# Optimization experiments

Hardware: AMD Instinct MI355X
Metric: run time of the kernel (lower is better)

The kernel has to match this reference:

```python
import jax, jax.numpy as jnp
import numpy as np

B, QN, KN, DIN, DPROJ = 8, 2048, 2048, 1024, 1024

def setup_inputs() -> dict:
    key = jax.random.key(0)
    ks = jax.random.split(key, 10)
    s = 1.0 / np.sqrt(DIN)
    return {
        "query": jax.random.normal(ks[0], (B, QN, DIN), jnp.float32),
        "key": jax.random.normal(ks[1], (B, KN, DIN), jnp.float32),
        "value": jax.random.normal(ks[2], (B, KN, DIN), jnp.float32),
        "mask": jax.random.randint(ks[3], (B, KN), 0, 2, jnp.int32),
        "Wq": jax.random.uniform(ks[4], (DPROJ, DIN), jnp.float32, -s, s),
        "bq": jax.random.uniform(ks[5], (DPROJ,), jnp.float32, -s, s),
        "Wk": jax.random.uniform(ks[6], (DPROJ, DIN), jnp.float32, -s, s),
        "bk": jax.random.uniform(ks[7], (DPROJ,), jnp.float32, -s, s),
        "Wv": jax.random.uniform(ks[8], (DPROJ, DIN), jnp.float32, -s, s),
        "bv": jax.random.uniform(ks[9], (DPROJ,), jnp.float32, -s, s),
    }

def reference(query, key, value, mask, Wq, bq, Wk, bk, Wv, bv):
    pq = jnp.einsum('bqc,dc->bqd', query, Wq) + bq  # (b, qn, dproj)
    pk = jnp.einsum('bkc,dc->bkd', key, Wk) + bk    # (b, kn, dproj)
    pv = jnp.einsum('bkc,dc->bkd', value, Wv) + bv  # (b, kn, dproj)
    scores = jnp.einsum('bqd,bkd->bqk', pq, pk) / jnp.sqrt(jnp.float32(DPROJ))
    m = mask[:, None, :]  # (b, 1, kn) broadcasts over qn
    scores = jnp.where(m == 0, jnp.float32(-1e9), scores)
    attn = jax.nn.softmax(scores, axis=-1)
    attn = attn * m.astype(attn.dtype)  # post-softmax double mask
    ctx = jnp.einsum('bqk,bkd->bqd', attn, pv)
    return (ctx, attn)
```

## Files before the change

### kernel.cpp

```cpp
#include <hip/hip_runtime.h>
#include <hip/hip_bf16.h>


typedef __bf16 bf16;
typedef __bf16 bf16x4 __attribute__((ext_vector_type(4)));
typedef __bf16 bf16x8 __attribute__((ext_vector_type(8)));
typedef float f32x4 __attribute__((ext_vector_type(4)));

#define BAR() asm volatile("s_barrier" ::: "memory")
#define WAIT_LGKM0() do { asm volatile("s_waitcnt lgkmcnt(0)" ::: "memory"); \
                          __builtin_amdgcn_sched_barrier(0); } while (0)

__device__ __forceinline__ void gld_lds16(const bf16* g, bf16* l) {
  __builtin_amdgcn_global_load_lds(
      (const __attribute__((address_space(1))) void*)g,
      (__attribute__((address_space(3))) void*)l, 16, 0, 0);
}

__global__ __launch_bounds__(256)
void cvt_f32_bf16(const float* __restrict__ src, bf16* __restrict__ dst, int n)
{
  long i = ((long)blockIdx.x * 256 + threadIdx.x) * 8;
  if (i >= n) return;
  f32x4 a = *(const f32x4*)&src[i];
  f32x4 b = *(const f32x4*)&src[i + 4];
  bf16x8 o;
  o[0] = (bf16)a[0]; o[1] = (bf16)a[1]; o[2] = (bf16)a[2]; o[3] = (bf16)a[3];
  o[4] = (bf16)b[0]; o[5] = (bf16)b[1]; o[6] = (bf16)b[2]; o[7] = (bf16)b[3];
  *(bf16x8*)&dst[i] = o;
}

__global__ __launch_bounds__(512, 2)
void gemm8p(const bf16* __restrict__ A, int lda, long sA,
            const bf16* __restrict__ Bt, int ldb, long sB,
            void* __restrict__ Cout, int ldc, long sC, int c_bf16,
            const float* __restrict__ bias, int bias_mode,
            int K, float scale)
{
  extern __shared__ bf16 lds[];
  const int tid = threadIdx.x;
  const int lane = tid & 63;
  const int wid = tid >> 6;
  const int wr = wid >> 2;
  const int wc = wid & 3;
  const long m0 = (long)blockIdx.x * 256;
  const long n0 = (long)blockIdx.y * 256;
  A  += (long)blockIdx.z * sA;
  Bt += (long)blockIdx.z * sB;

  const int fr = lane & 15, fq = lane >> 4;
  const int cs0 = (((fq * 16)      ^ ((fr & 7) << 4)) >> 1);
  const int cs1 = (((64 + fq * 16) ^ ((fr & 7) << 4)) >> 1);
  const int rbA = (wr * 128 + fr) * 64;
  const int rbB = 16384 + (wc * 64 + fr) * 64;

  const int srow = tid >> 3;
  const int slot = (tid & 7) ^ (srow & 7);
  const bf16* Ag[4]; const bf16* Bg[4];
#pragma unroll
  for (int h = 0; h < 2; ++h)
#pragma unroll
    for (int i = 0; i < 2; ++i) {
      Ag[h * 2 + i] = A  + (m0 + h * 128 + i * 64 + srow) * (long)lda + slot * 8;
      Bg[h * 2 + i] = Bt + (n0 + h * 128 + i * 64 + srow) * (long)ldb + slot * 8;
    }
  const int ldst = tid * 8;

  const int NT = K >> 6;
  f32x4 acc[8][4] = {};

#pragma unroll
  for (int hi = 0; hi < 4; ++hi)
    gld_lds16(Ag[hi], &lds[(hi >> 1) * 8192 + (hi & 1) * 4096 + ldst]);
#pragma unroll
  for (int hi = 0; hi < 4; ++hi)
    gld_lds16(Bg[hi], &lds[16384 + (hi >> 1) * 8192 + (hi & 1) * 4096 + ldst]);
#pragma unroll
  for (int hi = 0; hi < 4; ++hi)
    gld_lds16(Bg[hi] + 64, &lds[49152 + (hi >> 1) * 8192 + (hi & 1) * 4096 + ldst]);
  asm volatile("s_waitcnt vmcnt(4)" ::: "memory");
  BAR();

  for (int t = 0; t < NT; ++t) {
    const int bo  = (t & 1) << 15;
    const int nbo = bo ^ 32768;
    const int kof  = (t + 1) * 64;
    const int kof2 = (t + 2) * 64;
    const bool st1 = (t + 1 < NT), st2 = (t + 2 < NT);

    bf16x8 a0[4][2], b0[2][2], b1[2][2];

#pragma unroll
    for (int mf = 0; mf < 4; ++mf) {
      a0[mf][0] = *(const bf16x8*)&lds[bo + rbA + mf * 1024 + cs0];
      a0[mf][1] = *(const bf16x8*)&lds[bo + rbA + mf * 1024 + cs1];
    }
#pragma unroll
    for (int nf = 0; nf < 2; ++nf) {
      b0[nf][0] = *(const bf16x8*)&lds[bo + rbB + nf * 1024 + cs0];
      b0[nf][1] = *(const bf16x8*)&lds[bo + rbB + nf * 1024 + cs1];
    }
    if (st1) {
      gld_lds16(Ag[0] + kof, &lds[nbo + ldst]);
      gld_lds16(Ag[1] + kof, &lds[nbo + 4096 + ldst]);
    }
    BAR(); WAIT_LGKM0();
    __builtin_amdgcn_s_setprio(1);
#pragma unroll
    for (int mf = 0; mf < 4; ++mf)
#pragma unroll
      for (int nf = 0; nf < 2; ++nf) {
        acc[mf][nf] = __builtin_amdgcn_mfma_f32_16x16x32_bf16(a0[mf][0], b0[nf][0], acc[mf][nf], 0, 0, 0);
        acc[mf][nf] = __builtin_amdgcn_mfma_f32_16x16x32_bf16(a0[mf][1], b0[nf][1], acc[mf][nf], 0, 0, 0);
      }
    __builtin_amdgcn_s_setprio(0);
    BAR();

#pragma unroll
    for (int nf = 0; nf < 2; ++nf) {
      b1[nf][0] = *(const bf16x8*)&lds[bo + rbB + (nf + 2) * 1024 + cs0];
      b1[nf][1] = *(const bf16x8*)&lds[bo + rbB + (nf + 2) * 1024 + cs1];
    }
    if (st1) {
      gld_lds16(Ag[2] + kof, &lds[nbo + 8192 + ldst]);
      gld_lds16(Ag[3] + kof, &lds[nbo + 8192 + 4096 + ldst]);
    }
    BAR(); WAIT_LGKM0();
    __builtin_amdgcn_s_setprio(1);
#pragma unroll
    for (int mf = 0; mf < 4; ++mf)
#pragma unroll
      for (int nf = 0; nf < 2; ++nf) {
        acc[mf][nf + 2] = __builtin_amdgcn_mfma_f32_16x16x32_bf16(a0[mf][0], b1[nf][0], acc[mf][nf + 2], 0, 0, 0);
        acc[mf][nf + 2] = __builtin_amdgcn_mfma_f32_16x16x32_bf16(a0[mf][1], b1[nf][1], acc[mf][nf + 2], 0, 0, 0);
      }
    __builtin_amdgcn_s_setprio(0);
    BAR();

#pragma unroll
    for (int mf = 0; mf < 4; ++mf) {
      a0[mf][0] = *(const bf16x8*)&lds[bo + rbA + (mf + 4) * 1024 + cs0];
      a0[mf][1] = *(const bf16x8*)&lds[bo + rbA + (mf + 4) * 1024 + cs1];
    }
    if (st2) {
      gld_lds16(Bg[0] + kof2, &lds[bo + 16384 + ldst]);
      gld_lds16(Bg[1] + kof2, &lds[bo + 16384 + 4096 + ldst]);
    }
    BAR(); WAIT_LGKM0();
    __builtin_amdgcn_s_setprio(1);
#pragma unroll
    for (int mf = 0; mf < 4; ++mf)
#pragma unroll
      for (int nf = 0; nf < 2; ++nf) {
        acc[mf + 4][nf + 2] = __builtin_amdgcn_mfma_f32_16x16x32_bf16(a0[mf][0], b1[nf][0], acc[mf + 4][nf + 2], 0, 0, 0);
        acc[mf + 4][nf + 2] = __builtin_amdgcn_mfma_f32_16x16x32_bf16(a0[mf][1], b1[nf][1], acc[mf + 4][nf + 2], 0, 0, 0);
      }
    __builtin_amdgcn_s_setprio(0);
    BAR();

    if (st2) {
      gld_lds16(Bg[2] + kof2, &lds[bo + 16384 + 8192 + ldst]);
      gld_lds16(Bg[3] + kof2, &lds[bo + 16384 + 8192 + 4096 + ldst]);
      asm volatile("s_waitcnt vmcnt(4)" ::: "memory");
    } else {
      asm volatile("s_waitcnt vmcnt(0)" ::: "memory");
    }
    BAR(); WAIT_LGKM0();
    __builtin_amdgcn_s_setprio(1);
#pragma unroll
    for (int mf = 0; mf < 4; ++mf)
#pragma unroll
      for (int nf = 0; nf < 2; ++nf) {
        acc[mf + 4][nf] = __builtin_amdgcn_mfma_f32_16x16x32_bf16(a0[mf][0], b0[nf][0], acc[mf + 4][nf], 0, 0, 0);
        acc[mf + 4][nf] = __builtin_amdgcn_mfma_f32_16x16x32_bf16(a0[mf][1], b0[nf][1], acc[mf + 4][nf], 0, 0, 0);
      }
    __builtin_amdgcn_s_setprio(0);
    BAR();
  }

  const int cc = lane & 15, cq = lane >> 4;
  const long crow0 = m0 + wr * 128;
  const long ccol0 = n0 + wc * 64;
  if (c_bf16) {
    bf16* C = (bf16*)Cout + (long)blockIdx.z * sC;
#pragma unroll
    for (int mf = 0; mf < 8; ++mf)
#pragma unroll
      for (int nf = 0; nf < 4; ++nf)
#pragma unroll
        for (int r = 0; r < 4; ++r) {
          long row = crow0 + mf * 16 + cq * 4 + r;
          long col = ccol0 + nf * 16 + cc;
          float v = acc[mf][nf][r] * scale;
          if (bias_mode == 1) v += bias[col];
          else if (bias_mode == 2) v += bias[row];
          C[row * (long)ldc + col] = (bf16)v;
        }
  } else {
    float* C = (float*)Cout + (long)blockIdx.z * sC;
#pragma unroll
    for (int mf = 0; mf < 8; ++mf)
#pragma unroll
      for (int nf = 0; nf < 4; ++nf)
#pragma unroll
        for (int r = 0; r < 4; ++r) {
          long row = crow0 + mf * 16 + cq * 4 + r;
          long col = ccol0 + nf * 16 + cc;
          float v = acc[mf][nf][r] * scale;
          if (bias_mode == 1) v += bias[col];
          else if (bias_mode == 2) v += bias[row];
          C[row * (long)ldc + col] = v;
        }
  }
}

__global__ __launch_bounds__(256)
void softmax_mask(const int* __restrict__ mask, float* __restrict__ attn,
                  bf16* __restrict__ attnb)
{
  const int row = blockIdx.x;
  const int b = row >> 11;
  float* arow = attn + (long)row * 2048;
  const bf16* srow_b = (const bf16*)arow;
  bf16* brow = attnb + (long)row * 2048;
  const int* mrow = mask + (b << 11);
  const int tid = threadIdx.x;
  const int lane = tid & 63, wave = tid >> 6;

  bf16x4 sb[2];
  int4 mk[2];
  sb[0] = *(const bf16x4*)&srow_b[tid * 4];
  sb[1] = *(const bf16x4*)&srow_b[1024 + tid * 4];
  mk[0] = *(const int4*)&mrow[tid * 4];
  mk[1] = *(const int4*)&mrow[1024 + tid * 4];
  const int m[8] = {mk[0].x, mk[0].y, mk[0].z, mk[0].w,
                    mk[1].x, mk[1].y, mk[1].z, mk[1].w};
  float s[8];
#pragma unroll
  for (int i = 0; i < 8; ++i) s[i] = (float)sb[i >> 2][i & 3];

  float mx = -3e38f;
#pragma unroll
  for (int i = 0; i < 8; ++i)
    if (m[i]) mx = fmaxf(mx, s[i]);
#pragma unroll
  for (int off = 32; off > 0; off >>= 1) mx = fmaxf(mx, __shfl_xor(mx, off));
  __shared__ float rmax[4], rsum[4];
  if (lane == 0) rmax[wave] = mx;
  __syncthreads();
  mx = fmaxf(fmaxf(rmax[0], rmax[1]), fmaxf(rmax[2], rmax[3]));

  float e[8], sum = 0.f;
#pragma unroll
  for (int i = 0; i < 8; ++i) {
    e[i] = m[i] ? __expf(s[i] - mx) : 0.f;
    sum += e[i];
  }
#pragma unroll
  for (int off = 32; off > 0; off >>= 1) sum += __shfl_xor(sum, off);
  if (lane == 0) rsum[wave] = sum;
  __syncthreads();
  sum = rsum[0] + rsum[1] + rsum[2] + rsum[3];
  float inv = sum > 0.f ? 1.f / sum : 0.f;

  f32x4 o; bf16x4 ob;
#pragma unroll
  for (int h = 0; h < 2; ++h) {
#pragma unroll
    for (int i = 0; i < 4; ++i) {
      float v = e[h * 4 + i] * inv;
      o[i] = v; ob[i] = (bf16)v;
    }
    *(f32x4*)&arow[h * 1024 + tid * 4] = o;
    *(bf16x4*)&brow[h * 1024 + tid * 4] = ob;
  }
}

extern "C" void kernel_launch(void* const* d_in, const int* in_sizes, int n_in,
                              void* d_out, int out_size, void* d_ws, size_t ws_size,
                              hipStream_t stream)
{
  const float* query = (const float*)d_in[0];
  const float* key   = (const float*)d_in[1];
  const float* value = (const float*)d_in[2];
  const int*   mask  = (const int*)d_in[3];
  const float* Wq = (const float*)d_in[4];
  const float* bq = (const float*)d_in[5];
  const float* Wk = (const float*)d_in[6];
  const float* bk = (const float*)d_in[7];
  const float* Wv = (const float*)d_in[8];
  const float* bv = (const float*)d_in[9];

  float* ctx  = (float*)d_out;
  float* attn = ctx + (size_t)8 * 2048 * 1024;

  bf16* Pq    = (bf16*)d_ws;
  bf16* Pk    = Pq + (size_t)16384 * 1024;
  bf16* PvT   = Pk + (size_t)16384 * 1024;
  bf16* attnb = (bf16*)d_ws;

  bf16* qb  = (bf16*)attn;
  bf16* kb  = qb + (size_t)16384 * 1024;
  bf16* vb  = kb + (size_t)16384 * 1024;
  bf16* Wqb = vb + (size_t)16384 * 1024;
  bf16* Wkb = Wqb + (size_t)1024 * 1024;
  bf16* Wvb = Wkb + (size_t)1024 * 1024;

  static bool attr_set = false;
  if (!attr_set) {
    hipFuncSetAttribute(reinterpret_cast<const void*>(gemm8p),
                        hipFuncAttributeMaxDynamicSharedMemorySize, 131072);
    attr_set = true;
  }

  dim3 blk(256), blk8(512);

  hipLaunchKernelGGL(cvt_f32_bf16, dim3(8192), blk, 0, stream, query, qb, 16384 * 1024);
  hipLaunchKernelGGL(cvt_f32_bf16, dim3(8192), blk, 0, stream, key,   kb, 16384 * 1024);
  hipLaunchKernelGGL(cvt_f32_bf16, dim3(8192), blk, 0, stream, value, vb, 16384 * 1024);
  hipLaunchKernelGGL(cvt_f32_bf16, dim3(512),  blk, 0, stream, Wq, Wqb, 1024 * 1024);
  hipLaunchKernelGGL(cvt_f32_bf16, dim3(512),  blk, 0, stream, Wk, Wkb, 1024 * 1024);
  hipLaunchKernelGGL(cvt_f32_bf16, dim3(512),  blk, 0, stream, Wv, Wvb, 1024 * 1024);

  hipLaunchKernelGGL(gemm8p, dim3(64, 4, 1), blk8, 131072, stream,
      qb, 1024, 0L, Wqb, 1024, 0L, (void*)Pq, 1024, 0L, 1, bq, 1, 1024, 1.0f);
  hipLaunchKernelGGL(gemm8p, dim3(64, 4, 1), blk8, 131072, stream,
      kb, 1024, 0L, Wkb, 1024, 0L, (void*)Pk, 1024, 0L, 1, bk, 1, 1024, 1.0f);
  hipLaunchKernelGGL(gemm8p, dim3(4, 64, 1), blk8, 131072, stream,
      Wvb, 1024, 0L, vb, 1024, 0L, (void*)PvT, 16384, 0L, 1, bv, 2, 1024, 1.0f);
  hipLaunchKernelGGL(gemm8p, dim3(8, 8, 8), blk8, 131072, stream,
      Pq, 1024, (long)2048 * 1024, Pk, 1024, (long)2048 * 1024,
      (void*)attn, 4096, (long)2048 * 4096, 1, (const float*)nullptr, 0, 1024, 0.03125f);
  hipLaunchKernelGGL(softmax_mask, dim3(16384), blk, 0, stream, mask, attn, attnb);
  hipLaunchKernelGGL(gemm8p, dim3(8, 4, 8), blk8, 131072, stream,
      attnb, 2048, (long)2048 * 2048, PvT, 16384, 2048L,
      (void*)ctx, 1024, (long)2048 * 1024, 0, (const float*)nullptr, 0, 2048, 1.0f);
}
```

Baseline: 681.7 us.

## Restructure GEMM main loop into two phases and merge conversion launches

The GEMM K-loop goes from four barrier-separated MFMA phases to two. Each phase loads all four A or B fragment pairs, issues all four half-tile global-to-LDS prefetches at once, and waits partially on lgkmcnt before the barrier. This cuts barriers and gives longer MFMA runs, at the cost of more live fragment registers under the 512-thread, 2-block occupancy bound. The six fp32-to-bf16 conversion launches are merged into one kernel that dispatches on a flat index, removing launch overhead.

```diff
diff --git a/kernel.cpp b/kernel.cpp
--- a/kernel.cpp
+++ b/kernel.cpp
@@ -17,17 +17,30 @@
       (__attribute__((address_space(3))) void*)l, 16, 0, 0);
 }
 
-__global__ __launch_bounds__(256)
-void cvt_f32_bf16(const float* __restrict__ src, bf16* __restrict__ dst, int n)
-{
-  long i = ((long)blockIdx.x * 256 + threadIdx.x) * 8;
-  if (i >= n) return;
-  f32x4 a = *(const f32x4*)&src[i];
-  f32x4 b = *(const f32x4*)&src[i + 4];
+__device__ __forceinline__ void cvt8(const float* s, bf16* d, long i) {
+  f32x4 a = *(const f32x4*)&s[i];
+  f32x4 b = *(const f32x4*)&s[i + 4];
   bf16x8 o;
   o[0] = (bf16)a[0]; o[1] = (bf16)a[1]; o[2] = (bf16)a[2]; o[3] = (bf16)a[3];
   o[4] = (bf16)b[0]; o[5] = (bf16)b[1]; o[6] = (bf16)b[2]; o[7] = (bf16)b[3];
-  *(bf16x8*)&dst[i] = o;
+  *(bf16x8*)&d[i] = o;
+}
+
+__global__ __launch_bounds__(256)
+void cvt_all(const float* __restrict__ s0, bf16* __restrict__ d0, long n0,
+             const float* __restrict__ s1, bf16* __restrict__ d1, long n1,
+             const float* __restrict__ s2, bf16* __restrict__ d2, long n2,
+             const float* __restrict__ s3, bf16* __restrict__ d3, long n3,
+             const float* __restrict__ s4, bf16* __restrict__ d4, long n4,
+             const float* __restrict__ s5, bf16* __restrict__ d5, long n5)
+{
+  long g = ((long)blockIdx.x * 256 + threadIdx.x) * 8;
+  if (g < n0) { cvt8(s0, d0, g); return; } g -= n0;
+  if (g < n1) { cvt8(s1, d1, g); return; } g -= n1;
+  if (g < n2) { cvt8(s2, d2, g); return; } g -= n2;
+  if (g < n3) { cvt8(s3, d3, g); return; } g -= n3;
+  if (g < n4) { cvt8(s4, d4, g); return; } g -= n4;
+  if (g < n5) { cvt8(s5, d5, g); return; }
 }
 
 __global__ __launch_bounds__(512, 2)
@@ -58,12 +71,10 @@
   const int slot = (tid & 7) ^ (srow & 7);
   const bf16* Ag[4]; const bf16* Bg[4];
 #pragma unroll
-  for (int h = 0; h < 2; ++h)
-#pragma unroll
-    for (int i = 0; i < 2; ++i) {
-      Ag[h * 2 + i] = A  + (m0 + h * 128 + i * 64 + srow) * (long)lda + slot * 8;
-      Bg[h * 2 + i] = Bt + (n0 + h * 128 + i * 64 + srow) * (long)ldb + slot * 8;
-    }
+  for (int hi = 0; hi < 4; ++hi) {
+    Ag[hi] = A  + (m0 + hi * 64 + srow) * (long)lda + slot * 8;
+    Bg[hi] = Bt + (n0 + hi * 64 + srow) * (long)ldb + slot * 8;
+  }
   const int ldst = tid * 8;
 
   const int NT = K >> 6;
@@ -71,13 +82,13 @@
 
 #pragma unroll
   for (int hi = 0; hi < 4; ++hi)
-    gld_lds16(Ag[hi], &lds[(hi >> 1) * 8192 + (hi & 1) * 4096 + ldst]);
+    gld_lds16(Ag[hi], &lds[hi * 4096 + ldst]);
 #pragma unroll
   for (int hi = 0; hi < 4; ++hi)
-    gld_lds16(Bg[hi], &lds[16384 + (hi >> 1) * 8192 + (hi & 1) * 4096 + ldst]);
+    gld_lds16(Bg[hi], &lds[16384 + hi * 4096 + ldst]);
 #pragma unroll
   for (int hi = 0; hi < 4; ++hi)
-    gld_lds16(Bg[hi] + 64, &lds[49152 + (hi >> 1) * 8192 + (hi & 1) * 4096 + ldst]);
+    gld_lds16(Bg[hi] + 64, &lds[49152 + hi * 4096 + ldst]);
   asm volatile("s_waitcnt vmcnt(4)" ::: "memory");
   BAR();
 
@@ -88,79 +99,47 @@
     const int kof2 = (t + 2) * 64;
     const bool st1 = (t + 1 < NT), st2 = (t + 2 < NT);
 
-    bf16x8 a0[4][2], b0[2][2], b1[2][2];
-
+    bf16x8 a[4][2], b[4][2];
+
+    if (st1) {
+#pragma unroll
+      for (int hi = 0; hi < 4; ++hi)
+        gld_lds16(Ag[hi] + kof, &lds[nbo + hi * 4096 + ldst]);
+    }
 #pragma unroll
     for (int mf = 0; mf < 4; ++mf) {
-      a0[mf][0] = *(const bf16x8*)&lds[bo + rbA + mf * 1024 + cs0];
-      a0[mf][1] = *(const bf16x8*)&lds[bo + rbA + mf * 1024 + cs1];
-    }
-#pragma unroll
-    for (int nf = 0; nf < 2; ++nf) {
-      b0[nf][0] = *(const bf16x8*)&lds[bo + rbB + nf * 1024 + cs0];
-      b0[nf][1] = *(const bf16x8*)&lds[bo + rbB + nf * 1024 + cs1];
-    }
-    if (st1) {
-      gld_lds16(Ag[0] + kof, &lds[nbo + ldst]);
-      gld_lds16(Ag[1] + kof, &lds[nbo + 4096 + ldst]);
-    }
+      a[mf][0] = *(const bf16x8*)&lds[bo + rbA + mf * 1024 + cs0];
+      a[mf][1] = *(const bf16x8*)&lds[bo + rbA + mf * 1024 + cs1];
+    }
+#pragma unroll
+    for (int nf = 0; nf < 4; ++nf) {
+      b[nf][0] = *(const bf16x8*)&lds[bo + rbB + nf * 1024 + cs0];
+      b[nf][1] = *(const bf16x8*)&lds[bo + rbB + nf * 1024 + cs1];
+    }
+    asm volatile("s_waitcnt lgkmcnt(8)" ::: "memory");
     BAR(); WAIT_LGKM0();
     __builtin_amdgcn_s_setprio(1);
 #pragma unroll
     for (int mf = 0; mf < 4; ++mf)
 #pragma unroll
-      for (int nf = 0; nf < 2; ++nf) {
-        acc[mf][nf] = __builtin_amdgcn_mfma_f32_16x16x32_bf16(a0[mf][0], b0[nf][0], acc[mf][nf], 0, 0, 0);
-        acc[mf][nf] = __builtin_amdgcn_mfma_f32_16x16x32_bf16(a0[mf][1], b0[nf][1], acc[mf][nf], 0, 0, 0);
+      for (int nf = 0; nf < 4; ++nf) {
+        acc[mf][nf] = __builtin_amdgcn_mfma_f32_16x16x32_bf16(a[mf][0], b[nf][0], acc[mf][nf], 0, 0, 0);
+        acc[mf][nf] = __builtin_amdgcn_mfma_f32_16x16x32_bf16(a[mf][1], b[nf][1], acc[mf][nf], 0, 0, 0);
       }
     __builtin_amdgcn_s_setprio(0);
     BAR();
 
-#pragma unroll
-    for (int nf = 0; nf < 2; ++nf) {
-      b1[nf][0] = *(const bf16x8*)&lds[bo + rbB + (nf + 2) * 1024 + cs0];
-      b1[nf][1] = *(const bf16x8*)&lds[bo + rbB + (nf + 2) * 1024 + cs1];
-    }
-    if (st1) {
-      gld_lds16(Ag[2] + kof, &lds[nbo + 8192 + ldst]);
-      gld_lds16(Ag[3] + kof, &lds[nbo + 8192 + 4096 + ldst]);
-    }
-    BAR(); WAIT_LGKM0();
-    __builtin_amdgcn_s_setprio(1);
-#pragma unroll
-    for (int mf = 0; mf < 4; ++mf)
-#pragma unroll
-      for (int nf = 0; nf < 2; ++nf) {
-        acc[mf][nf + 2] = __builtin_amdgcn_mfma_f32_16x16x32_bf16(a0[mf][0], b1[nf][0], acc[mf][nf + 2], 0, 0, 0);
-        acc[mf][nf + 2] = __builtin_amdgcn_mfma_f32_16x16x32_bf16(a0[mf][1], b1[nf][1], acc[mf][nf + 2], 0, 0, 0);
-      }
-    __builtin_amdgcn_s_setprio(0);
-    BAR();
-
+    if (st2) {
+#pragma unroll
+      for (int hi = 0; hi < 4; ++hi)
+        gld_lds16(Bg[hi] + kof2, &lds[bo + 16384 + hi * 4096 + ldst]);
+    }
 #pragma unroll
     for (int mf = 0; mf < 4; ++mf) {
-      a0[mf][0] = *(const bf16x8*)&lds[bo + rbA + (mf + 4) * 1024 + cs0];
-      a0[mf][1] = *(const bf16x8*)&lds[bo + rbA + (mf + 4) * 1024 + cs1];
+      a[mf][0] = *(const bf16x8*)&lds[bo + rbA + (mf + 4) * 1024 + cs0];
+      a[mf][1] = *(const bf16x8*)&lds[bo + rbA + (mf + 4) * 1024 + cs1];
     }
     if (st2) {
-      gld_lds16(Bg[0] + kof2, &lds[bo + 16384 + ldst]);
-      gld_lds16(Bg[1] + kof2, &lds[bo + 16384 + 4096 + ldst]);
-    }
-    BAR(); WAIT_LGKM0();
-    __builtin_amdgcn_s_setprio(1);
-#pragma unroll
-    for (int mf = 0; mf < 4; ++mf)
-#pragma unroll
-      for (int nf = 0; nf < 2; ++nf) {
-        acc[mf + 4][nf + 2] = __builtin_amdgcn_mfma_f32_16x16x32_bf16(a0[mf][0], b1[nf][0], acc[mf + 4][nf + 2], 0, 0, 0);
-        acc[mf + 4][nf + 2] = __builtin_amdgcn_mfma_f32_16x16x32_bf16(a0[mf][1], b1[nf][1], acc[mf + 4][nf + 2], 0, 0, 0);
-      }
-    __builtin_amdgcn_s_setprio(0);
-    BAR();
-
-    if (st2) {
-      gld_lds16(Bg[2] + kof2, &lds[bo + 16384 + 8192 + ldst]);
-      gld_lds16(Bg[3] + kof2, &lds[bo + 16384 + 8192 + 4096 + ldst]);
       asm volatile("s_waitcnt vmcnt(4)" ::: "memory");
     } else {
       asm volatile("s_waitcnt vmcnt(0)" ::: "memory");
@@ -170,9 +149,9 @@
 #pragma unroll
     for (int mf = 0; mf < 4; ++mf)
 #pragma unroll
-      for (int nf = 0; nf < 2; ++nf) {
-        acc[mf + 4][nf] = __builtin_amdgcn_mfma_f32_16x16x32_bf16(a0[mf][0], b0[nf][0], acc[mf + 4][nf], 0, 0, 0);
-        acc[mf + 4][nf] = __builtin_amdgcn_mfma_f32_16x16x32_bf16(a0[mf][1], b0[nf][1], acc[mf + 4][nf], 0, 0, 0);
+      for (int nf = 0; nf < 4; ++nf) {
+        acc[mf + 4][nf] = __builtin_amdgcn_mfma_f32_16x16x32_bf16(a[mf][0], b[nf][0], acc[mf + 4][nf], 0, 0, 0);
+        acc[mf + 4][nf] = __builtin_amdgcn_mfma_f32_16x16x32_bf16(a[mf][1], b[nf][1], acc[mf + 4][nf], 0, 0, 0);
       }
     __builtin_amdgcn_s_setprio(0);
     BAR();
@@ -314,13 +293,11 @@
   }
 
   dim3 blk(256), blk8(512);
-
-  hipLaunchKernelGGL(cvt_f32_bf16, dim3(8192), blk, 0, stream, query, qb, 16384 * 1024);
-  hipLaunchKernelGGL(cvt_f32_bf16, dim3(8192), blk, 0, stream, key,   kb, 16384 * 1024);
-  hipLaunchKernelGGL(cvt_f32_bf16, dim3(8192), blk, 0, stream, value, vb, 16384 * 1024);
-  hipLaunchKernelGGL(cvt_f32_bf16, dim3(512),  blk, 0, stream, Wq, Wqb, 1024 * 1024);
-  hipLaunchKernelGGL(cvt_f32_bf16, dim3(512),  blk, 0, stream, Wk, Wkb, 1024 * 1024);
-  hipLaunchKernelGGL(cvt_f32_bf16, dim3(512),  blk, 0, stream, Wv, Wvb, 1024 * 1024);
+  const long NQ = 16384L * 1024, NW = 1024L * 1024;
+
+  hipLaunchKernelGGL(cvt_all, dim3(26112), blk, 0, stream,
+      query, qb, NQ, key, kb, NQ, value, vb, NQ,
+      Wq, Wqb, NW, Wk, Wkb, NW, Wv, Wvb, NW);
 
   hipLaunchKernelGGL(gemm8p, dim3(64, 4, 1), blk8, 131072, stream,
       qb, 1024, 0L, Wqb, 1024, 0L, (void*)Pq, 1024, 0L, 1, bq, 1, 1024, 1.0f);
```

After: 672.3 us. No clear change (-1.4%).
